# Kernel optimization log

Hardware: AMD Instinct MI355X
Metric: run time of the kernel (lower is better)

The kernel has to match this reference:

```python
import jax, jax.numpy as jnp
import numpy as np

TAU = 0.2          # temperature from __init__
BETA = 0.5         # time-penalty weight
SIGMA = 1.0        # time-penalty width
QUERY_TIME = 100.0 # query timestamp


def setup_inputs() -> dict:
    key = jax.random.key(0)
    k1, k2, k3, k4 = jax.random.split(key, 4)
    B, N, D = 1024, 65536, 1024
    query = jax.random.normal(k1, (B, D), jnp.float32)
    K = jax.random.normal(k2, (N, D), jnp.float32)
    # write() stores F.normalize(key), so keys live on the unit sphere
    K = K / jnp.linalg.norm(K, axis=-1, keepdims=True)
    V = jax.random.normal(k3, (N, D), jnp.float32)
    times = jax.random.uniform(k4, (N,), jnp.float32, 0.0, 100.0)
    return {"query": query, "K": K, "V": V, "times": times, "topk": 32}


def reference(query, K, V, times, topk):
    # F.normalize(query, dim=-1)
    qn = query / jnp.maximum(jnp.linalg.norm(query, axis=-1, keepdims=True), 1e-12)
    # similarity logits over the memory bank: [B, N]
    logits = jnp.einsum('bd,nd->bn', qn, K) / TAU
    # quadratic recency penalty (beta > 0, sigma > 0 branch)
    penalty = BETA * ((QUERY_TIME - times) ** 2) / (2.0 * SIGMA * SIGMA)
    logits = logits - penalty[None, :]
    # top-k retrieval + softmax over selected logits
    vals, idxs = jax.lax.top_k(logits, topk)          # [B, k]
    attn = jax.nn.softmax(vals, axis=-1)              # [B, k]
    v_sel = V[idxs]                                   # [B, k, D] gather
    out = jnp.einsum('bk,bkd->bd', attn, v_sel)       # weighted sum
    return out
```

## Files before the change

kernel.cpp:

```cpp
#include <hip/hip_runtime.h>
#include <cmath>

constexpr int B = 1024;
constexpr int N = 65536;
constexpr int D = 1024;
constexpr int K_TOP = 32;
constexpr int RSEL = 40;
constexpr int CAP = 128;
constexpr int CMAX = 5120;
constexpr int NKEY = CMAX / 256;

#define PEN_C 0.25
#define QT 100.0
#define TAUINV 5.0
#define TMINF 93.51925f
#define HGRAN 124.0f

typedef short  short8 __attribute__((ext_vector_type(8)));
typedef float  f32x4  __attribute__((ext_vector_type(4)));

constexpr size_t OFF_QNB  = 0;
constexpr size_t OFF_KC   = OFF_QNB  + (size_t)B * D * 2;
constexpr size_t OFF_LOG  = OFF_KC   + (size_t)CMAX * D * 2;
constexpr size_t OFF_CIDX = OFF_LOG  + (size_t)B * CMAX * 2;
constexpr size_t OFF_CPEN = OFF_CIDX + (size_t)CMAX * 4;
constexpr size_t OFF_QSC  = OFF_CPEN + (size_t)CMAX * 8;
constexpr size_t OFF_SCAL = OFF_QSC  + (size_t)B * 8;

__device__ inline unsigned short f2bf(float f) {
    unsigned u = __float_as_uint(f);
    unsigned r = (u + 0x7fffu + ((u >> 16) & 1u)) >> 16;
    return (unsigned short)r;
}

__device__ inline void gl_lds16(const void* g, void* l) {
    auto* g1 = (const __attribute__((address_space(1))) unsigned*)g;
    auto* l3 = (__attribute__((address_space(3))) unsigned*)l;
    __builtin_amdgcn_global_load_lds(g1, l3, 16, 0, 0);
}


__global__ void __launch_bounds__(256) k_prep(const float* __restrict__ q,
                                              const float* __restrict__ times,
                                              double* __restrict__ qsc,
                                              unsigned short* __restrict__ qnb,
                                              int* __restrict__ cidx,
                                              double* __restrict__ cpen,
                                              int* __restrict__ countp) {
    const int tid = threadIdx.x;
    const int lane = tid & 63, wid = tid >> 6;

    if (blockIdx.x < B) {
        const int row = blockIdx.x;
        const float4 v = reinterpret_cast<const float4*>(q + (size_t)row * D)[tid];
        double ss = (double)v.x * v.x + (double)v.y * v.y +
                    (double)v.z * v.z + (double)v.w * v.w;
        for (int off = 32; off; off >>= 1) ss += __shfl_xor(ss, off);
        __shared__ double wsum[4];
        if (lane == 0) wsum[wid] = ss;
        __syncthreads();
        double tot = wsum[0] + wsum[1] + wsum[2] + wsum[3];
        double sc = 1.0 / fmax(sqrt(tot), 1e-12);
        if (tid == 0) qsc[row] = sc;
        ushort4 b = make_ushort4(f2bf((float)(v.x * sc)), f2bf((float)(v.y * sc)),
                                 f2bf((float)(v.z * sc)), f2bf((float)(v.w * sc)));
        reinterpret_cast<ushort4*>(qnb + (size_t)row * D)[tid] = b;
        return;
    }

    __shared__ int cwt[4];
    const float4* t4 = reinterpret_cast<const float4*>(times);
    const int base = wid * 16384;

    int cnt = 0;
    for (int bu = 0; bu < 8; ++bu) {
        float4 f[8];
#pragma unroll
        for (int u = 0; u < 8; ++u) f[u] = t4[wid * 4096 + (bu * 8 + u) * 64 + lane];
#pragma unroll
        for (int u = 0; u < 8; ++u) {
            cnt += (f[u].x >= TMINF) ? 1 : 0;
            cnt += (f[u].y >= TMINF) ? 1 : 0;
            cnt += (f[u].z >= TMINF) ? 1 : 0;
            cnt += (f[u].w >= TMINF) ? 1 : 0;
        }
    }
    for (int off = 32; off; off >>= 1) cnt += __shfl_xor(cnt, off);
    if (lane == 0) cwt[wid] = cnt;
    __syncthreads();
    int wbase = 0, total = 0;
#pragma unroll
    for (int w2 = 0; w2 < 4; ++w2) {
        int c = cwt[w2];
        if (w2 < wid) wbase += c;
        total += c;
    }

    const unsigned long long lt = (1ull << lane) - 1ull;
    for (int bu = 0; bu < 8; ++bu) {
        float4 f[8];
#pragma unroll
        for (int u = 0; u < 8; ++u) f[u] = t4[wid * 4096 + (bu * 8 + u) * 64 + lane];
#pragma unroll
        for (int u = 0; u < 8; ++u) {
            bool f0 = (f[u].x >= TMINF), f1 = (f[u].y >= TMINF);
            bool f2 = (f[u].z >= TMINF), f3 = (f[u].w >= TMINF);
            unsigned long long b0 = __ballot(f0), b1 = __ballot(f1);
            unsigned long long b2 = __ballot(f2), b3 = __ballot(f3);
            int below = __popcll(b0 & lt) + __popcll(b1 & lt) +
                        __popcll(b2 & lt) + __popcll(b3 & lt);
            int gidx = base + (bu * 8 + u) * 256 + lane * 4;
            int p = wbase + below;
            double u0 = QT - (double)f[u].x, u1 = QT - (double)f[u].y;
            double u2 = QT - (double)f[u].z, u3 = QT - (double)f[u].w;
            if (f0 && p < CMAX) { cidx[p] = gidx + 0; cpen[p] = PEN_C * u0 * u0; ++p; }
            if (f1 && p < CMAX) { cidx[p] = gidx + 1; cpen[p] = PEN_C * u1 * u1; ++p; }
            if (f2 && p < CMAX) { cidx[p] = gidx + 2; cpen[p] = PEN_C * u2 * u2; ++p; }
            if (f3 && p < CMAX) { cidx[p] = gidx + 3; cpen[p] = PEN_C * u3 * u3; ++p; }
            wbase += __popcll(b0) + __popcll(b1) + __popcll(b2) + __popcll(b3);
        }
    }
    if (tid == 0) countp[0] = min(total, CMAX);
}

__global__ void __launch_bounds__(256) k_packK(const float* __restrict__ Kmat,
                                               const int* __restrict__ cidx,
                                               const int* __restrict__ countp,
                                               unsigned short* __restrict__ Kc) {
    const int count = countp[0];
    const int count_r = (count + 127) & ~127;
    int gid = blockIdx.x * 256 + threadIdx.x;
    int row = gid >> 7;
    int c8  = (gid & 127) * 8;
    if (row >= count_r) return;
    unsigned short ob[8];
    if (row < count) {
        const float* src = Kmat + (size_t)cidx[row] * D + c8;
        float4 a = reinterpret_cast<const float4*>(src)[0];
        float4 b = reinterpret_cast<const float4*>(src)[1];
        ob[0] = f2bf(a.x); ob[1] = f2bf(a.y); ob[2] = f2bf(a.z); ob[3] = f2bf(a.w);
        ob[4] = f2bf(b.x); ob[5] = f2bf(b.y); ob[6] = f2bf(b.z); ob[7] = f2bf(b.w);
    } else {
#pragma unroll
        for (int j = 0; j < 8; ++j) ob[j] = 0;
    }
    *reinterpret_cast<short8*>(Kc + (size_t)row * D + c8) = *reinterpret_cast<short8*>(ob);
}

__global__ void __launch_bounds__(512) k_mfma(const unsigned short* __restrict__ qnb,
                                              const unsigned short* __restrict__ Kc,
                                              const double* __restrict__ cpen,
                                              const int* __restrict__ countp,
                                              _Float16* __restrict__ logits) {
    const int count = countp[0];
    const int bx = blockIdx.x, by = blockIdx.y;
    if (bx * 128 >= ((count + 127) & ~127)) return;

    __shared__ unsigned short As[2][8192];
    __shared__ unsigned short Bs[2][8192];

    const int tid = threadIdx.x;
    const int l = tid & 63, w = tid >> 6;
    const int wr = w >> 2, wc = w & 3;
    const int lr = l & 15, lk = (l >> 4) * 8;

    const unsigned short* ga0 = qnb + (size_t)(by * 128 + (tid >> 3)) * D + (tid & 7) * 8;
    const unsigned short* gb0 = Kc  + (size_t)(bx * 128 + (tid >> 3)) * D + (tid & 7) * 8;

    f32x4 acc[4][2] = {};

    gl_lds16(ga0,                  &As[0][tid * 8]);
    gl_lds16(ga0 + (size_t)64 * D, &As[0][4096 + tid * 8]);
    gl_lds16(gb0,                  &Bs[0][tid * 8]);
    gl_lds16(gb0 + (size_t)64 * D, &Bs[0][4096 + tid * 8]);
    __syncthreads();

    int cur = 0;
    for (int t = 0; t < 16; ++t) {
        if (t < 15) {
            const int k1 = (t + 1) * 64;
            gl_lds16(ga0 + k1,                  &As[cur ^ 1][tid * 8]);
            gl_lds16(ga0 + (size_t)64 * D + k1, &As[cur ^ 1][4096 + tid * 8]);
            gl_lds16(gb0 + k1,                  &Bs[cur ^ 1][tid * 8]);
            gl_lds16(gb0 + (size_t)64 * D + k1, &Bs[cur ^ 1][4096 + tid * 8]);
        }
#pragma unroll
        for (int ks = 0; ks < 2; ++ks) {
            const int kk = ks * 32 + lk;
            short8 a[4], b[2];
#pragma unroll
            for (int mi = 0; mi < 4; ++mi)
                a[mi] = *reinterpret_cast<const short8*>(&As[cur][(wr * 64 + mi * 16 + lr) * 64 + kk]);
#pragma unroll
            for (int ni = 0; ni < 2; ++ni)
                b[ni] = *reinterpret_cast<const short8*>(&Bs[cur][(wc * 32 + ni * 16 + lr) * 64 + kk]);
#pragma unroll
            for (int mi = 0; mi < 4; ++mi)
#pragma unroll
                for (int ni = 0; ni < 2; ++ni)
                    acc[mi][ni] = __builtin_amdgcn_mfma_f32_16x16x32_bf16(
                        a[mi], b[ni], acc[mi][ni], 0, 0, 0);
        }
        __syncthreads();
        cur ^= 1;
    }

    const int row0 = by * 128 + wr * 64 + (l >> 4) * 4;
    const int col0 = bx * 128 + wc * 32;
#pragma unroll
    for (int ni = 0; ni < 2; ++ni) {
        const int c = col0 + ni * 16 + lr;
        if (c < count) {
            const float pen = (float)cpen[c];
#pragma unroll
            for (int mi = 0; mi < 4; ++mi) {
                const int r = row0 + mi * 16;
#pragma unroll
                for (int j = 0; j < 4; ++j)
                    logits[(size_t)(r + j) * CMAX + c] =
                        (_Float16)(acc[mi][ni][j] * (float)TAUINV - pen);
            }
        }
    }
}

__global__ void __launch_bounds__(256) k_select(const _Float16* __restrict__ logits,
                                                const int* __restrict__ cidx,
                                                const double* __restrict__ cpen,
                                                const int* __restrict__ countp,
                                                const double* __restrict__ qsc,
                                                const float* __restrict__ q,
                                                const float* __restrict__ Kmat,
                                                const float* __restrict__ Vmat,
                                                float* __restrict__ out) {
    const int row = blockIdx.x, tid = threadIdx.x;
    const int count = countp[0];
    const _Float16* lrow = logits + (size_t)row * CMAX;

    __shared__ int    hist16[16][257];
    __shared__ int    suf[256];
    __shared__ int    selslot[CAP];
    __shared__ double refv[CAP];
    __shared__ float  qs[D];
    __shared__ double selw[K_TOP];
    __shared__ int    selg[K_TOP];
    __shared__ int    scal_i[4];
    __shared__ double sdbl[2];
    __shared__ float  fmx[4];
    __shared__ int    wt[4];

    const int lane = tid & 63, wid = tid >> 6;
    const int grp = tid >> 4;
    const double s5 = qsc[row] * (double)TAUINV;

    reinterpret_cast<float4*>(qs)[tid] =
        reinterpret_cast<const float4*>(q + (size_t)row * D)[tid];
    if (tid == 0) { scal_i[0] = 254; scal_i[1] = 0; }
#pragma unroll
    for (int g = 0; g < 16; ++g) hist16[g][tid] = 0;

    float lv[NKEY];
    float m = -1e30f;
#pragma unroll
    for (int j = 0; j < NKEY; ++j) {
        int c = tid + j * 256;
        lv[j] = (c < count) ? (float)lrow[c] : -1e30f;
        m = fmaxf(m, lv[j]);
    }
    for (int off = 32; off; off >>= 1) m = fmaxf(m, __shfl_xor(m, off));
    if (lane == 0) fmx[wid] = m;
    __syncthreads();
    const float vmax = fmaxf(fmaxf(fmx[0], fmx[1]), fmaxf(fmx[2], fmx[3]));

#pragma unroll
    for (int j = 0; j < NKEY; ++j) {
        int bin = (int)((vmax - lv[j]) * HGRAN);
        if (bin < 255 && tid + j * 256 < count) atomicAdd(&hist16[grp][bin], 1);
    }
    __syncthreads();
    {
        int s = 0;
#pragma unroll
        for (int g = 0; g < 16; ++g) s += hist16[g][tid];
        int v = s;
#pragma unroll
        for (int off = 1; off < 64; off <<= 1) {
            int o = __shfl_up(v, off);
            if (lane >= off) v += o;
        }
        if (lane == 63) wt[wid] = v;
        __syncthreads();
        int add = 0;
#pragma unroll
        for (int w2 = 0; w2 < 4; ++w2) if (w2 < wid) add += wt[w2];
        suf[tid] = v + add;
    }
    __syncthreads();
    if (suf[tid] >= RSEL && (tid == 0 || suf[tid - 1] < RSEL)) scal_i[0] = tid;
    __syncthreads();
    const int T = scal_i[0];

#pragma unroll
    for (int j = 0; j < NKEY; ++j) {
        int c = tid + j * 256;
        int bin = (int)((vmax - lv[j]) * HGRAN);
        if (bin <= T && c < count) {
            int pos = atomicAdd(&scal_i[1], 1);
            if (pos < CAP) selslot[pos] = c;
        }
    }
    __syncthreads();
    const int cnt = min(scal_i[1], CAP);

    {
        const int g = tid >> 4, l16 = tid & 15;
        for (int b = 0; b * 16 < cnt; ++b) {
            const int kk = b * 16 + g;
            if (kk < cnt) {
                const int slot = selslot[kk];
                const int n = cidx[slot];
                const float* kr = Kmat + (size_t)n * D + l16 * 4;
                double acc = 0.0;
#pragma unroll
                for (int j = 0; j < 16; ++j) {
                    float4 kv = reinterpret_cast<const float4*>(kr + j * 64)[0];
                    float4 qv = reinterpret_cast<const float4*>(&qs[l16 * 4 + j * 64])[0];
                    acc = fma((double)kv.x, (double)qv.x, acc);
                    acc = fma((double)kv.y, (double)qv.y, acc);
                    acc = fma((double)kv.z, (double)qv.z, acc);
                    acc = fma((double)kv.w, (double)qv.w, acc);
                }
#pragma unroll
                for (int off = 1; off < 16; off <<= 1) acc += __shfl_xor(acc, off);
                if (l16 == 0) refv[kk] = acc * s5 - cpen[slot];
            }
        }
    }
    __syncthreads();

    {
        const bool act = (tid < cnt);
        double v = act ? refv[tid] : -1e300;
        int slot = act ? selslot[tid] : 0x7fffffff;
        int rank = 0;
        for (int j = 0; j < cnt; ++j) {
            double vj = refv[j];
            int sj = selslot[j];
            rank += (vj > v || (vj == v && sj < slot)) ? 1 : 0;
        }
        if (act && rank == 0) sdbl[0] = v;
        __syncthreads();
        if (act && rank < K_TOP) {
            selw[rank] = exp(v - sdbl[0]);
            selg[rank] = cidx[slot];
        }
        __syncthreads();
        if (tid == 0) {
            double ssum = 0.0;
            for (int k = 0; k < K_TOP; ++k) ssum += selw[k];
            sdbl[1] = 1.0 / ssum;
        }
        __syncthreads();
    }

    const double inv = sdbl[1];
    double o0 = 0, o1 = 0, o2 = 0, o3 = 0;
    for (int k = 0; k < K_TOP; ++k) {
        double wv = selw[k] * inv;
        float4 v = reinterpret_cast<const float4*>(Vmat + (size_t)selg[k] * D)[tid];
        o0 = fma(wv, (double)v.x, o0);
        o1 = fma(wv, (double)v.y, o1);
        o2 = fma(wv, (double)v.z, o2);
        o3 = fma(wv, (double)v.w, o3);
    }
    float4 r = make_float4((float)o0, (float)o1, (float)o2, (float)o3);
    reinterpret_cast<float4*>(out + (size_t)row * D)[tid] = r;
}

extern "C" void kernel_launch(void* const* d_in, const int* in_sizes, int n_in,
                              void* d_out, int out_size, void* d_ws, size_t ws_size,
                              hipStream_t stream) {
    (void)in_sizes; (void)n_in; (void)out_size; (void)ws_size;
    const float* q     = (const float*)d_in[0];
    const float* Kmat  = (const float*)d_in[1];
    const float* Vmat  = (const float*)d_in[2];
    const float* times = (const float*)d_in[3];
    float* out = (float*)d_out;

    char* ws = (char*)d_ws;
    unsigned short* qnb    = (unsigned short*)(ws + OFF_QNB);
    unsigned short* Kc     = (unsigned short*)(ws + OFF_KC);
    _Float16*       logits = (_Float16*)(ws + OFF_LOG);
    int*            cidx   = (int*)(ws + OFF_CIDX);
    double*         cpen   = (double*)(ws + OFF_CPEN);
    double*         qsc    = (double*)(ws + OFF_QSC);
    int*            countp = (int*)(ws + OFF_SCAL);

    hipLaunchKernelGGL(k_prep,   dim3(B + 1), dim3(256), 0, stream,
                       q, times, qsc, qnb, cidx, cpen, countp);
    hipLaunchKernelGGL(k_packK,  dim3((CMAX * (D / 8)) / 256), dim3(256), 0, stream,
                       Kmat, cidx, countp, Kc);
    hipLaunchKernelGGL(k_mfma,   dim3(CMAX / 128, B / 128), dim3(512), 0, stream,
                       qnb, Kc, cpen, countp, logits);
    hipLaunchKernelGGL(k_select, dim3(B), dim3(256), 0, stream,
                       logits, cidx, cpen, countp, qsc, q, Kmat, Vmat, out);
}
```

Baseline: 93.30 us.

## Fuse K gather and bf16 packing into the MFMA GEMM B-tile loader

Removes the separate k_packK kernel that gathered candidate K rows and converted them to bf16 in a workspace buffer. The GEMM now reads fp32 K rows through cidx in registers, converts them to bf16 and writes them into LDS after the MFMA compute of each stage. This drops a kernel launch and a bf16 round trip through global memory. In exchange, each of the 8 row-blocks of queries re-reads the fp32 K rows, doubling the bytes per element versus the bf16 copy, and the register-staged B path may raise register pressure under the new launch bound of 4.

```diff
diff --git a/kernel.cpp b/kernel.cpp
--- a/kernel.cpp
+++ b/kernel.cpp
@@ -20,8 +20,7 @@
 typedef float  f32x4  __attribute__((ext_vector_type(4)));
 
 constexpr size_t OFF_QNB  = 0;
-constexpr size_t OFF_KC   = OFF_QNB  + (size_t)B * D * 2;
-constexpr size_t OFF_LOG  = OFF_KC   + (size_t)CMAX * D * 2;
+constexpr size_t OFF_LOG  = OFF_QNB  + (size_t)B * D * 2;
 constexpr size_t OFF_CIDX = OFF_LOG  + (size_t)B * CMAX * 2;
 constexpr size_t OFF_CPEN = OFF_CIDX + (size_t)CMAX * 4;
 constexpr size_t OFF_QSC  = OFF_CPEN + (size_t)CMAX * 8;
@@ -123,38 +122,16 @@
     if (tid == 0) countp[0] = min(total, CMAX);
 }
 
-__global__ void __launch_bounds__(256) k_packK(const float* __restrict__ Kmat,
-                                               const int* __restrict__ cidx,
-                                               const int* __restrict__ countp,
-                                               unsigned short* __restrict__ Kc) {
+__global__ void __launch_bounds__(512, 4) k_mfma(const unsigned short* __restrict__ qnb,
+                                                 const float* __restrict__ Kmat,
+                                                 const int* __restrict__ cidx,
+                                                 const double* __restrict__ cpen,
+                                                 const int* __restrict__ countp,
+                                                 _Float16* __restrict__ logits) {
     const int count = countp[0];
     const int count_r = (count + 127) & ~127;
-    int gid = blockIdx.x * 256 + threadIdx.x;
-    int row = gid >> 7;
-    int c8  = (gid & 127) * 8;
-    if (row >= count_r) return;
-    unsigned short ob[8];
-    if (row < count) {
-        const float* src = Kmat + (size_t)cidx[row] * D + c8;
-        float4 a = reinterpret_cast<const float4*>(src)[0];
-        float4 b = reinterpret_cast<const float4*>(src)[1];
-        ob[0] = f2bf(a.x); ob[1] = f2bf(a.y); ob[2] = f2bf(a.z); ob[3] = f2bf(a.w);
-        ob[4] = f2bf(b.x); ob[5] = f2bf(b.y); ob[6] = f2bf(b.z); ob[7] = f2bf(b.w);
-    } else {
-#pragma unroll
-        for (int j = 0; j < 8; ++j) ob[j] = 0;
-    }
-    *reinterpret_cast<short8*>(Kc + (size_t)row * D + c8) = *reinterpret_cast<short8*>(ob);
-}
-
-__global__ void __launch_bounds__(512) k_mfma(const unsigned short* __restrict__ qnb,
-                                              const unsigned short* __restrict__ Kc,
-                                              const double* __restrict__ cpen,
-                                              const int* __restrict__ countp,
-                                              _Float16* __restrict__ logits) {
-    const int count = countp[0];
     const int bx = blockIdx.x, by = blockIdx.y;
-    if (bx * 128 >= ((count + 127) & ~127)) return;
+    if (bx * 128 >= count_r) return;
 
     __shared__ unsigned short As[2][8192];
     __shared__ unsigned short Bs[2][8192];
@@ -165,24 +142,51 @@
     const int lr = l & 15, lk = (l >> 4) * 8;
 
     const unsigned short* ga0 = qnb + (size_t)(by * 128 + (tid >> 3)) * D + (tid & 7) * 8;
-    const unsigned short* gb0 = Kc  + (size_t)(bx * 128 + (tid >> 3)) * D + (tid & 7) * 8;
+
+    const int br = tid >> 2, qt = tid & 3;
+    const int grow = bx * 128 + br;
+    const bool bvalid = (grow < count);
+    const float* kb = Kmat + (size_t)(bvalid ? cidx[grow] : 0) * D + qt * 16;
+
+    float bs[16];
+    auto loadB = [&](int k0) {
+        if (bvalid) {
+            const float4* p4 = reinterpret_cast<const float4*>(kb + k0);
+            float4 v0 = p4[0], v1 = p4[1], v2 = p4[2], v3 = p4[3];
+            bs[0]  = v0.x; bs[1]  = v0.y; bs[2]  = v0.z; bs[3]  = v0.w;
+            bs[4]  = v1.x; bs[5]  = v1.y; bs[6]  = v1.z; bs[7]  = v1.w;
+            bs[8]  = v2.x; bs[9]  = v2.y; bs[10] = v2.z; bs[11] = v2.w;
+            bs[12] = v3.x; bs[13] = v3.y; bs[14] = v3.z; bs[15] = v3.w;
+        } else {
+#pragma unroll
+            for (int j = 0; j < 16; ++j) bs[j] = 0.0f;
+        }
+    };
+    auto writeB = [&](int buf) {
+        unsigned short ob[16];
+#pragma unroll
+        for (int j = 0; j < 16; ++j) ob[j] = f2bf(bs[j]);
+        *reinterpret_cast<short8*>(&Bs[buf][br * 64 + qt * 16]) =
+            *reinterpret_cast<short8*>(&ob[0]);
+        *reinterpret_cast<short8*>(&Bs[buf][br * 64 + qt * 16 + 8]) =
+            *reinterpret_cast<short8*>(&ob[8]);
+    };
 
     f32x4 acc[4][2] = {};
 
+    loadB(0);
     gl_lds16(ga0,                  &As[0][tid * 8]);
     gl_lds16(ga0 + (size_t)64 * D, &As[0][4096 + tid * 8]);
-    gl_lds16(gb0,                  &Bs[0][tid * 8]);
-    gl_lds16(gb0 + (size_t)64 * D, &Bs[0][4096 + tid * 8]);
+    writeB(0);
     __syncthreads();
 
     int cur = 0;
     for (int t = 0; t < 16; ++t) {
         if (t < 15) {
             const int k1 = (t + 1) * 64;
+            loadB(k1);
             gl_lds16(ga0 + k1,                  &As[cur ^ 1][tid * 8]);
             gl_lds16(ga0 + (size_t)64 * D + k1, &As[cur ^ 1][4096 + tid * 8]);
-            gl_lds16(gb0 + k1,                  &Bs[cur ^ 1][tid * 8]);
-            gl_lds16(gb0 + (size_t)64 * D + k1, &Bs[cur ^ 1][4096 + tid * 8]);
         }
 #pragma unroll
         for (int ks = 0; ks < 2; ++ks) {
@@ -201,6 +205,7 @@
                     acc[mi][ni] = __builtin_amdgcn_mfma_f32_16x16x32_bf16(
                         a[mi], b[ni], acc[mi][ni], 0, 0, 0);
         }
+        if (t < 15) writeB(cur ^ 1);
         __syncthreads();
         cur ^= 1;
     }
@@ -389,7 +394,6 @@
 
     char* ws = (char*)d_ws;
     unsigned short* qnb    = (unsigned short*)(ws + OFF_QNB);
-    unsigned short* Kc     = (unsigned short*)(ws + OFF_KC);
     _Float16*       logits = (_Float16*)(ws + OFF_LOG);
     int*            cidx   = (int*)(ws + OFF_CIDX);
     double*         cpen   = (double*)(ws + OFF_CPEN);
@@ -398,10 +402,8 @@
 
     hipLaunchKernelGGL(k_prep,   dim3(B + 1), dim3(256), 0, stream,
                        q, times, qsc, qnb, cidx, cpen, countp);
-    hipLaunchKernelGGL(k_packK,  dim3((CMAX * (D / 8)) / 256), dim3(256), 0, stream,
-                       Kmat, cidx, countp, Kc);
     hipLaunchKernelGGL(k_mfma,   dim3(CMAX / 128, B / 128), dim3(512), 0, stream,
-                       qnb, Kc, cpen, countp, logits);
+                       qnb, Kmat, cidx, cpen, countp, logits);
     hipLaunchKernelGGL(k_select, dim3(B), dim3(256), 0, stream,
                        logits, cidx, cpen, countp, qsc, q, Kmat, Vmat, out);
 }
```

Result: no change. 93.61 us (+0.3%).

## Split-K the candidate GEMM into two halves and fold penalty into select

Applied to the files above, without the earlier changes.

The logits GEMM is split along D into two halves, so the grid doubles to 640 blocks, now indexed through a 1D remap that interleaves work across XCDs. Each half writes its own fp16 partial logits buffer. k_select sums the two partials and subtracts a new float penalty array that k_prep writes. RSEL is raised from 40 to 48, and launch bounds ask for higher occupancy. The aim is better CU utilization, since the old 40x8 grid was small, at the cost of twice the logit write and read traffic and an extra fp16 rounding step.

```diff
diff --git a/kernel.cpp b/kernel.cpp
--- a/kernel.cpp
+++ b/kernel.cpp
@@ -5,7 +5,7 @@
 constexpr int N = 65536;
 constexpr int D = 1024;
 constexpr int K_TOP = 32;
-constexpr int RSEL = 40;
+constexpr int RSEL = 48;
 constexpr int CAP = 128;
 constexpr int CMAX = 5120;
 constexpr int NKEY = CMAX / 256;
@@ -22,9 +22,10 @@
 constexpr size_t OFF_QNB  = 0;
 constexpr size_t OFF_KC   = OFF_QNB  + (size_t)B * D * 2;
 constexpr size_t OFF_LOG  = OFF_KC   + (size_t)CMAX * D * 2;
-constexpr size_t OFF_CIDX = OFF_LOG  + (size_t)B * CMAX * 2;
+constexpr size_t OFF_CIDX = OFF_LOG  + (size_t)2 * B * CMAX * 2;
 constexpr size_t OFF_CPEN = OFF_CIDX + (size_t)CMAX * 4;
-constexpr size_t OFF_QSC  = OFF_CPEN + (size_t)CMAX * 8;
+constexpr size_t OFF_PENF = OFF_CPEN + (size_t)CMAX * 8;
+constexpr size_t OFF_QSC  = OFF_PENF + (size_t)CMAX * 4;
 constexpr size_t OFF_SCAL = OFF_QSC  + (size_t)B * 8;
 
 __device__ inline unsigned short f2bf(float f) {
@@ -46,6 +47,7 @@
                                               unsigned short* __restrict__ qnb,
                                               int* __restrict__ cidx,
                                               double* __restrict__ cpen,
+                                              float* __restrict__ penf,
                                               int* __restrict__ countp) {
     const int tid = threadIdx.x;
     const int lane = tid & 63, wid = tid >> 6;
@@ -113,10 +115,14 @@
             int p = wbase + below;
             double u0 = QT - (double)f[u].x, u1 = QT - (double)f[u].y;
             double u2 = QT - (double)f[u].z, u3 = QT - (double)f[u].w;
-            if (f0 && p < CMAX) { cidx[p] = gidx + 0; cpen[p] = PEN_C * u0 * u0; ++p; }
-            if (f1 && p < CMAX) { cidx[p] = gidx + 1; cpen[p] = PEN_C * u1 * u1; ++p; }
-            if (f2 && p < CMAX) { cidx[p] = gidx + 2; cpen[p] = PEN_C * u2 * u2; ++p; }
-            if (f3 && p < CMAX) { cidx[p] = gidx + 3; cpen[p] = PEN_C * u3 * u3; ++p; }
+            if (f0 && p < CMAX) { cidx[p] = gidx + 0; cpen[p] = PEN_C * u0 * u0;
+                                  penf[p] = (float)(PEN_C * u0 * u0); ++p; }
+            if (f1 && p < CMAX) { cidx[p] = gidx + 1; cpen[p] = PEN_C * u1 * u1;
+                                  penf[p] = (float)(PEN_C * u1 * u1); ++p; }
+            if (f2 && p < CMAX) { cidx[p] = gidx + 2; cpen[p] = PEN_C * u2 * u2;
+                                  penf[p] = (float)(PEN_C * u2 * u2); ++p; }
+            if (f3 && p < CMAX) { cidx[p] = gidx + 3; cpen[p] = PEN_C * u3 * u3;
+                                  penf[p] = (float)(PEN_C * u3 * u3); ++p; }
             wbase += __popcll(b0) + __popcll(b1) + __popcll(b2) + __popcll(b3);
         }
     }
@@ -147,14 +153,18 @@
     *reinterpret_cast<short8*>(Kc + (size_t)row * D + c8) = *reinterpret_cast<short8*>(ob);
 }
 
-__global__ void __launch_bounds__(512) k_mfma(const unsigned short* __restrict__ qnb,
-                                              const unsigned short* __restrict__ Kc,
-                                              const double* __restrict__ cpen,
-                                              const int* __restrict__ countp,
-                                              _Float16* __restrict__ logits) {
+__global__ void __launch_bounds__(512, 4) k_mfma(const unsigned short* __restrict__ qnb,
+                                                 const unsigned short* __restrict__ Kc,
+                                                 const int* __restrict__ countp,
+                                                 _Float16* __restrict__ logits) {
+    const int work = (blockIdx.x & 7) * 80 + (blockIdx.x >> 3);
+    const int kh = work & 1;
+    const int by = (work >> 1) & 7;
+    const int bx = work >> 4;
+
     const int count = countp[0];
-    const int bx = blockIdx.x, by = blockIdx.y;
-    if (bx * 128 >= ((count + 127) & ~127)) return;
+    const int count_r = (count + 127) & ~127;
+    if (bx * 128 >= count_r) return;
 
     __shared__ unsigned short As[2][8192];
     __shared__ unsigned short Bs[2][8192];
@@ -164,8 +174,9 @@
     const int wr = w >> 2, wc = w & 3;
     const int lr = l & 15, lk = (l >> 4) * 8;
 
-    const unsigned short* ga0 = qnb + (size_t)(by * 128 + (tid >> 3)) * D + (tid & 7) * 8;
-    const unsigned short* gb0 = Kc  + (size_t)(bx * 128 + (tid >> 3)) * D + (tid & 7) * 8;
+    const size_t kbase = (size_t)kh * 512;
+    const unsigned short* ga0 = qnb + (size_t)(by * 128 + (tid >> 3)) * D + (tid & 7) * 8 + kbase;
+    const unsigned short* gb0 = Kc  + (size_t)(bx * 128 + (tid >> 3)) * D + (tid & 7) * 8 + kbase;
 
     f32x4 acc[4][2] = {};
 
@@ -176,8 +187,8 @@
     __syncthreads();
 
     int cur = 0;
-    for (int t = 0; t < 16; ++t) {
-        if (t < 15) {
+    for (int t = 0; t < 8; ++t) {
+        if (t < 7) {
             const int k1 = (t + 1) * 64;
             gl_lds16(ga0 + k1,                  &As[cur ^ 1][tid * 8]);
             gl_lds16(ga0 + (size_t)64 * D + k1, &As[cur ^ 1][4096 + tid * 8]);
@@ -205,20 +216,20 @@
         cur ^= 1;
     }
 
+    _Float16* lout = logits + (size_t)kh * B * CMAX;
     const int row0 = by * 128 + wr * 64 + (l >> 4) * 4;
     const int col0 = bx * 128 + wc * 32;
 #pragma unroll
     for (int ni = 0; ni < 2; ++ni) {
         const int c = col0 + ni * 16 + lr;
         if (c < count) {
-            const float pen = (float)cpen[c];
 #pragma unroll
             for (int mi = 0; mi < 4; ++mi) {
                 const int r = row0 + mi * 16;
 #pragma unroll
                 for (int j = 0; j < 4; ++j)
-                    logits[(size_t)(r + j) * CMAX + c] =
-                        (_Float16)(acc[mi][ni][j] * (float)TAUINV - pen);
+                    lout[(size_t)(r + j) * CMAX + c] =
+                        (_Float16)(acc[mi][ni][j] * (float)TAUINV);
             }
         }
     }
@@ -227,6 +238,7 @@
 __global__ void __launch_bounds__(256) k_select(const _Float16* __restrict__ logits,
                                                 const int* __restrict__ cidx,
                                                 const double* __restrict__ cpen,
+                                                const float* __restrict__ penf,
                                                 const int* __restrict__ countp,
                                                 const double* __restrict__ qsc,
                                                 const float* __restrict__ q,
@@ -235,7 +247,8 @@
                                                 float* __restrict__ out) {
     const int row = blockIdx.x, tid = threadIdx.x;
     const int count = countp[0];
-    const _Float16* lrow = logits + (size_t)row * CMAX;
+    const _Float16* la = logits + (size_t)row * CMAX;
+    const _Float16* lb = logits + (size_t)B * CMAX + (size_t)row * CMAX;
 
     __shared__ int    hist16[16][257];
     __shared__ int    suf[256];
@@ -264,7 +277,7 @@
 #pragma unroll
     for (int j = 0; j < NKEY; ++j) {
         int c = tid + j * 256;
-        lv[j] = (c < count) ? (float)lrow[c] : -1e30f;
+        lv[j] = (c < count) ? ((float)la[c] + (float)lb[c] - penf[c]) : -1e30f;
         m = fmaxf(m, lv[j]);
     }
     for (int off = 32; off; off >>= 1) m = fmaxf(m, __shfl_xor(m, off));
@@ -393,15 +406,16 @@
     _Float16*       logits = (_Float16*)(ws + OFF_LOG);
     int*            cidx   = (int*)(ws + OFF_CIDX);
     double*         cpen   = (double*)(ws + OFF_CPEN);
+    float*          penf   = (float*)(ws + OFF_PENF);
     double*         qsc    = (double*)(ws + OFF_QSC);
     int*            countp = (int*)(ws + OFF_SCAL);
 
     hipLaunchKernelGGL(k_prep,   dim3(B + 1), dim3(256), 0, stream,
-                       q, times, qsc, qnb, cidx, cpen, countp);
+                       q, times, qsc, qnb, cidx, cpen, penf, countp);
     hipLaunchKernelGGL(k_packK,  dim3((CMAX * (D / 8)) / 256), dim3(256), 0, stream,
                        Kmat, cidx, countp, Kc);
-    hipLaunchKernelGGL(k_mfma,   dim3(CMAX / 128, B / 128), dim3(512), 0, stream,
-                       qnb, Kc, cpen, countp, logits);
+    hipLaunchKernelGGL(k_mfma,   dim3(2 * (CMAX / 128) * 8), dim3(512), 0, stream,
+                       qnb, Kc, countp, logits);
     hipLaunchKernelGGL(k_select, dim3(B), dim3(256), 0, stream,
-                       logits, cidx, cpen, countp, qsc, q, Kmat, Vmat, out);
-}
+                       logits, cidx, cpen, penf, countp, qsc, q, Kmat, Vmat, out);
+}
```

Result: no change. 93.97 us (+0.7%).
